# Optimization experiments

Hardware: AMD Instinct MI355X
Metric: run time of the kernel (lower is better)

## Reference

```python
import jax, jax.numpy as jnp
import numpy as np
from jax import lax

B, C, N = 8, 3, 65536
NUM_POINTS = 1024


def setup_inputs() -> dict:
    key = jax.random.key(0)
    points = jax.random.normal(key, (B, C, N), dtype=jnp.float32)
    return {"points": points}


def furthest_point_sampling(xyz, num_points):
    # xyz: (B, N, 3) -> indices (B, num_points), int32
    b, n, _ = xyz.shape
    init_idx = jnp.zeros((b,), dtype=jnp.int32)  # CUDA FPS seeds with index 0
    init_dists = jnp.full((b, n), 1e10, dtype=xyz.dtype)

    def step(carry, _):
        dists, last_idx = carry
        last_pt = jnp.take_along_axis(xyz, last_idx[:, None, None], axis=1)  # (B,1,3)
        d = jnp.sum(jnp.square(xyz - last_pt), axis=-1)  # (B,N) squared dist to newest pt
        dists = jnp.minimum(dists, d)
        nxt = jnp.argmax(dists, axis=-1).astype(jnp.int32)
        return (dists, nxt), nxt

    (_, _), rest = lax.scan(step, (init_dists, init_idx), None, length=num_points - 1)
    # rest: (num_points-1, B) -> (B, num_points)
    idx = jnp.concatenate([init_idx[None, :], rest], axis=0).T
    return idx


def reference(points):
    # points: (B, 3, N), channels-first as in the torch module
    xyz = jnp.transpose(points, (0, 2, 1))  # (B, N, 3)
    idx = furthest_point_sampling(xyz, NUM_POINTS)  # (B, num_points)
    # fps_gather_by_index: gather along point axis of (B, 3, N)
    new_points = jnp.take_along_axis(points, idx[:, None, :], axis=2)  # (B, 3, num_points)
    return new_points
```

## Files before the change

kernel.cpp:

```cpp
#include <hip/hip_runtime.h>


namespace {

constexpr int kB = 8;
constexpr int kN = 65536;
constexpr int kNP = 1024;
constexpr int kPB = 16;
constexpr int kThreads = 256;
constexpr int kPPT = kN / (kPB * kThreads);
constexpr int kGrp = kPPT / 4;
constexpr int kWaves = kThreads / 64;
constexpr int kRgn = 16;
constexpr int kRgnStride = 32;
constexpr int kBlocks = 256;

__device__ __forceinline__ unsigned long long shfl_xor_u64(unsigned long long v, int off) {
  return (unsigned long long)__shfl_xor((long long)v, off, 64);
}

__device__ __forceinline__ unsigned long long u64max(unsigned long long a,
                                                     unsigned long long b) {
  return a > b ? a : b;
}

__device__ __forceinline__ unsigned long long load_l2(const unsigned long long* p) {
  unsigned long long v;
  asm volatile("global_load_dwordx2 %0, %1, off sc0\n\ts_waitcnt vmcnt(0)"
               : "=v"(v)
               : "v"(p)
               : "memory");
  return v;
}

__device__ __forceinline__ void store_l2(unsigned long long* p, unsigned long long v) {
  asm volatile("global_store_dwordx2 %0, %1, off sc0" ::"v"(p), "v"(v) : "memory");
}

__global__ __launch_bounds__(kThreads) void fps_kernel(const float* __restrict__ pts,
                                                       float* __restrict__ out,
                                                       unsigned long long* __restrict__ slots,
                                                       unsigned* __restrict__ ctrl) {
  const int tid = threadIdx.x;
  const int lane = tid & 63;
  const int wave = tid >> 6;

  __shared__ int s_batch, s_slice;
  __shared__ unsigned long long s_wkey[kWaves];
  __shared__ unsigned s_win[2];
  __shared__ int s_hist[kNP];

  if (tid == 0) {
    unsigned xcc;
    asm volatile("s_getreg_b32 %0, hwreg(HW_REG_XCC_ID)" : "=s"(xcc));
    const int home = (int)(xcc & 7u);
    int batch = -1, slice = -1;
    const int pos = (int)atomicAdd(&ctrl[home], 1u);
    if (pos < kPB) {
      batch = home;
      slice = pos;
    }
    __hip_atomic_fetch_add(&ctrl[8], 1u, __ATOMIC_RELEASE, __HIP_MEMORY_SCOPE_AGENT);
    if (batch < 0) {
      while (__hip_atomic_load(&ctrl[8], __ATOMIC_ACQUIRE, __HIP_MEMORY_SCOPE_AGENT) <
             (unsigned)kBlocks) {
        __builtin_amdgcn_s_sleep(8);
      }
      int need = (int)atomicAdd(&ctrl[9], 1u);
      for (int j = 0; j < kB; ++j) {
        int have = (int)__hip_atomic_load(&ctrl[j], __ATOMIC_RELAXED, __HIP_MEMORY_SCOPE_AGENT);
        have = have > kPB ? kPB : have;
        const int vac = kPB - have;
        if (need < vac) {
          batch = j;
          slice = have + need;
          break;
        }
        need -= vac;
      }
    }
    s_batch = batch;
    s_slice = slice;
    s_win[0] = 0xFFFFFFFFu;
    s_win[1] = 0xFFFFFFFFu;
  }
  __syncthreads();

  const int batch = s_batch;
  const int slice = s_slice;
  if (batch < 0) return;

  const float* __restrict__ xb = pts + (size_t)batch * 3 * kN;
  const float* __restrict__ yb = xb + kN;
  const float* __restrict__ zb = xb + 2 * kN;

  const int sbase = slice * (kThreads * kPPT);
  const int base0 = sbase + tid * 4;
  float px[kPPT], py[kPPT], pz[kPPT], dist[kPPT];
#pragma unroll
  for (int g = 0; g < kGrp; ++g) {
    const int base = base0 + g * (kThreads * 4);
    const float4 vx = *reinterpret_cast<const float4*>(xb + base);
    const float4 vy = *reinterpret_cast<const float4*>(yb + base);
    const float4 vz = *reinterpret_cast<const float4*>(zb + base);
    px[g * 4 + 0] = vx.x; px[g * 4 + 1] = vx.y; px[g * 4 + 2] = vx.z; px[g * 4 + 3] = vx.w;
    py[g * 4 + 0] = vy.x; py[g * 4 + 1] = vy.y; py[g * 4 + 2] = vy.z; py[g * 4 + 3] = vy.w;
    pz[g * 4 + 0] = vz.x; pz[g * 4 + 1] = vz.y; pz[g * 4 + 2] = vz.z; pz[g * 4 + 3] = vz.w;
  }
#pragma unroll
  for (int k = 0; k < kPPT; ++k) dist[k] = 1e10f;

  float qx = xb[0], qy = yb[0], qz = zb[0];

  unsigned long long* const sb = slots + (size_t)batch * kRgn * kRgnStride;

  for (int it = 1; it < kNP; ++it) {
    float bd = -1.0f;
    int bi = 0;
#pragma unroll
    for (int g = 0; g < kGrp; ++g) {
#pragma unroll
      for (int j = 0; j < 4; ++j) {
        const int k = g * 4 + j;
        const float dx = px[k] - qx;
        const float dy = py[k] - qy;
        const float dz = pz[k] - qz;
        const float ss =
            __fadd_rn(__fadd_rn(__fmul_rn(dx, dx), __fmul_rn(dy, dy)), __fmul_rn(dz, dz));
        const float nd = fminf(dist[k], ss);
        dist[k] = nd;
        if (nd > bd) {
          bd = nd;
          bi = base0 + g * (kThreads * 4) + j;
        }
      }
    }

    unsigned long long key = ((unsigned long long)__float_as_uint(bd) << 32) |
                             ((unsigned long long)(0xFFFFu - (unsigned)bi) << 16) |
                             (unsigned long long)(unsigned)it;

#pragma unroll
    for (int off = 32; off > 0; off >>= 1) {
      key = u64max(key, shfl_xor_u64(key, off));
    }
    if (lane == 0) s_wkey[wave] = key;
    __syncthreads();

    int wi;
    if (wave == 0) {
      unsigned long long bk = s_wkey[lane & (kWaves - 1)];
#pragma unroll
      for (int off = 1; off < kWaves; off <<= 1) {
        bk = u64max(bk, shfl_xor_u64(bk, off));
      }

      unsigned long long* const rgn = sb + (size_t)(it & (kRgn - 1)) * kRgnStride;
      if (lane == 0) {
        store_l2(rgn + slice, bk);
        __hip_atomic_store(rgn + kPB + slice, bk, __ATOMIC_RELAXED,
                           __HIP_MEMORY_SCOPE_AGENT);
      }

      unsigned long long w;
      int round = 0;
      for (;;) {
        unsigned long long a = load_l2(rgn + (lane & (kPB - 1)));
        bool ok = (unsigned)(a & 0xFFFFull) == (unsigned)it;
        if (round >= 2 && !ok) {
          const unsigned long long fb = __hip_atomic_load(
              rgn + kPB + (lane & (kPB - 1)), __ATOMIC_RELAXED, __HIP_MEMORY_SCOPE_AGENT);
          if ((unsigned)(fb & 0xFFFFull) == (unsigned)it) {
            a = fb;
            ok = true;
          }
        }
        if (__all(ok)) {
          w = a;
          break;
        }
        ++round;
      }
#pragma unroll
      for (int off = 1; off < kPB; off <<= 1) {
        w = u64max(w, shfl_xor_u64(w, off));
      }
      wi = (int)(0xFFFFu - ((unsigned)(w >> 16) & 0xFFFFu));
      if (lane == 0) {
        s_hist[it] = wi;
        __hip_atomic_store(&s_win[it & 1], ((unsigned)wi << 16) | (unsigned)it,
                           __ATOMIC_RELAXED, __HIP_MEMORY_SCOPE_WORKGROUP);
      }
    } else {
      unsigned v;
      do {
        v = __hip_atomic_load(&s_win[it & 1], __ATOMIC_RELAXED, __HIP_MEMORY_SCOPE_WORKGROUP);
      } while ((v & 0xFFFFu) != (unsigned)it);
      wi = (int)(v >> 16);
    }

    const int wiu = __builtin_amdgcn_readfirstlane(wi);
    qx = xb[wiu];
    qy = yb[wiu];
    qz = zb[wiu];
  }

  __syncthreads();

  if (slice == 0) {
    float* __restrict__ ob = out + (size_t)batch * 3 * kNP;
    for (int j = tid; j < kNP; j += kThreads) {
      const int id = (j == 0) ? 0 : s_hist[j];
      ob[j] = xb[id];
      ob[kNP + j] = yb[id];
      ob[2 * kNP + j] = zb[id];
    }
  }
}

}

extern "C" void kernel_launch(void* const* d_in, const int* in_sizes, int n_in,
                              void* d_out, int out_size, void* d_ws, size_t ws_size,
                              hipStream_t stream) {
  (void)in_sizes;
  (void)n_in;
  (void)out_size;
  (void)ws_size;
  const float* pts = (const float*)d_in[0];
  float* out = (float*)d_out;
  unsigned* ctrl = (unsigned*)d_ws;
  unsigned long long* slots = (unsigned long long*)((char*)d_ws + 1024);
  hipMemsetAsync(d_ws, 0, 64, stream);
  fps_kernel<<<dim3(kBlocks), dim3(kThreads), 0, stream>>>(pts, out, slots, ctrl);
}
```

Measured before the change: 1.662 ms.

## Use DPP wave reductions and place exchange slots in output buffer

```diff
diff --git a/kernel.cpp b/kernel.cpp
--- a/kernel.cpp
+++ b/kernel.cpp
@@ -12,16 +12,33 @@
 constexpr int kGrp = kPPT / 4;
 constexpr int kWaves = kThreads / 64;
 constexpr int kRgn = 16;
-constexpr int kRgnStride = 32;
 constexpr int kBlocks = 256;
-
-__device__ __forceinline__ unsigned long long shfl_xor_u64(unsigned long long v, int off) {
-  return (unsigned long long)__shfl_xor((long long)v, off, 64);
-}
+constexpr unsigned kDoneTag = 0xD07Eu;
 
 __device__ __forceinline__ unsigned long long u64max(unsigned long long a,
                                                      unsigned long long b) {
   return a > b ? a : b;
+}
+
+template <int CTRL>
+__device__ __forceinline__ unsigned long long dpp_u64_zero(unsigned long long v) {
+  const unsigned lo =
+      (unsigned)__builtin_amdgcn_update_dpp(0, (int)(unsigned)v, CTRL, 0xf, 0xf, false);
+  const unsigned hi =
+      (unsigned)__builtin_amdgcn_update_dpp(0, (int)(unsigned)(v >> 32), CTRL, 0xf, 0xf, false);
+  return ((unsigned long long)hi << 32) | lo;
+}
+
+__device__ __forceinline__ unsigned long long wave_max_u64(unsigned long long v) {
+  v = u64max(v, dpp_u64_zero<0x111>(v));
+  v = u64max(v, dpp_u64_zero<0x112>(v));
+  v = u64max(v, dpp_u64_zero<0x114>(v));
+  v = u64max(v, dpp_u64_zero<0x118>(v));
+  v = u64max(v, dpp_u64_zero<0x142>(v));
+  v = u64max(v, dpp_u64_zero<0x143>(v));
+  const unsigned lo = (unsigned)__builtin_amdgcn_readlane((int)(unsigned)v, 63);
+  const unsigned hi = (unsigned)__builtin_amdgcn_readlane((int)(unsigned)(v >> 32), 63);
+  return ((unsigned long long)hi << 32) | lo;
 }
 
 __device__ __forceinline__ unsigned long long load_l2(const unsigned long long* p) {
@@ -39,7 +56,8 @@
 
 __global__ __launch_bounds__(kThreads) void fps_kernel(const float* __restrict__ pts,
                                                        float* __restrict__ out,
-                                                       unsigned long long* __restrict__ slots,
+                                                       unsigned long long* __restrict__ slotsB,
+                                                       unsigned long long* __restrict__ done,
                                                        unsigned* __restrict__ ctrl) {
   const int tid = threadIdx.x;
   const int lane = tid & 63;
@@ -94,6 +112,9 @@
   const float* __restrict__ yb = xb + kN;
   const float* __restrict__ zb = xb + 2 * kN;
 
+  unsigned long long* const lineA = (unsigned long long*)(out + (size_t)batch * 3 * kNP);
+  unsigned long long* const lineB = slotsB + (size_t)batch * kRgn * kPB;
+
   const int sbase = slice * (kThreads * kPPT);
   const int base0 = sbase + tid * 4;
   float px[kPPT], py[kPPT], pz[kPPT], dist[kPPT];
@@ -111,8 +132,6 @@
   for (int k = 0; k < kPPT; ++k) dist[k] = 1e10f;
 
   float qx = xb[0], qy = yb[0], qz = zb[0];
-
-  unsigned long long* const sb = slots + (size_t)batch * kRgn * kRgnStride;
 
   for (int it = 1; it < kNP; ++it) {
     float bd = -1.0f;
@@ -140,36 +159,30 @@
                              ((unsigned long long)(0xFFFFu - (unsigned)bi) << 16) |
                              (unsigned long long)(unsigned)it;
 
-#pragma unroll
-    for (int off = 32; off > 0; off >>= 1) {
-      key = u64max(key, shfl_xor_u64(key, off));
-    }
+    key = wave_max_u64(key);
     if (lane == 0) s_wkey[wave] = key;
     __syncthreads();
 
     int wi;
     if (wave == 0) {
       unsigned long long bk = s_wkey[lane & (kWaves - 1)];
-#pragma unroll
-      for (int off = 1; off < kWaves; off <<= 1) {
-        bk = u64max(bk, shfl_xor_u64(bk, off));
-      }
-
-      unsigned long long* const rgn = sb + (size_t)(it & (kRgn - 1)) * kRgnStride;
+      bk = wave_max_u64(bk);
+
+      const int rg = (it & (kRgn - 1)) * kPB;
       if (lane == 0) {
-        store_l2(rgn + slice, bk);
-        __hip_atomic_store(rgn + kPB + slice, bk, __ATOMIC_RELAXED,
+        store_l2(lineA + rg + slice, bk);
+        __hip_atomic_store(lineB + rg + slice, bk, __ATOMIC_RELAXED,
                            __HIP_MEMORY_SCOPE_AGENT);
       }
 
       unsigned long long w;
       int round = 0;
       for (;;) {
-        unsigned long long a = load_l2(rgn + (lane & (kPB - 1)));
+        unsigned long long a = load_l2(lineA + rg + (lane & (kPB - 1)));
         bool ok = (unsigned)(a & 0xFFFFull) == (unsigned)it;
-        if (round >= 2 && !ok) {
+        if (round >= 3 && !ok) {
           const unsigned long long fb = __hip_atomic_load(
-              rgn + kPB + (lane & (kPB - 1)), __ATOMIC_RELAXED, __HIP_MEMORY_SCOPE_AGENT);
+              lineB + rg + (lane & (kPB - 1)), __ATOMIC_RELAXED, __HIP_MEMORY_SCOPE_AGENT);
           if ((unsigned)(fb & 0xFFFFull) == (unsigned)it) {
             a = fb;
             ok = true;
@@ -181,10 +194,7 @@
         }
         ++round;
       }
-#pragma unroll
-      for (int off = 1; off < kPB; off <<= 1) {
-        w = u64max(w, shfl_xor_u64(w, off));
-      }
+      w = wave_max_u64(w);
       wi = (int)(0xFFFFu - ((unsigned)(w >> 16) & 0xFFFFu));
       if (lane == 0) {
         s_hist[it] = wi;
@@ -207,7 +217,22 @@
 
   __syncthreads();
 
+  if (tid == 0) {
+    __hip_atomic_store(&done[batch * kPB + slice],
+                       ((unsigned long long)slice << 32) | kDoneTag, __ATOMIC_RELEASE,
+                       __HIP_MEMORY_SCOPE_AGENT);
+  }
+
   if (slice == 0) {
+    if (wave == 0) {
+      unsigned long long d;
+      do {
+        d = __hip_atomic_load(&done[batch * kPB + (lane & (kPB - 1))], __ATOMIC_ACQUIRE,
+                              __HIP_MEMORY_SCOPE_AGENT);
+      } while (!__all((unsigned)(d & 0xFFFFull) == kDoneTag));
+    }
+    __syncthreads();
+
     float* __restrict__ ob = out + (size_t)batch * 3 * kNP;
     for (int j = tid; j < kNP; j += kThreads) {
       const int id = (j == 0) ? 0 : s_hist[j];
@@ -230,7 +255,8 @@
   const float* pts = (const float*)d_in[0];
   float* out = (float*)d_out;
   unsigned* ctrl = (unsigned*)d_ws;
-  unsigned long long* slots = (unsigned long long*)((char*)d_ws + 1024);
+  unsigned long long* slotsB = (unsigned long long*)((char*)d_ws + 1024);
+  unsigned long long* done = (unsigned long long*)((char*)d_ws + 32768);
   hipMemsetAsync(d_ws, 0, 64, stream);
-  fps_kernel<<<dim3(kBlocks), dim3(kThreads), 0, stream>>>(pts, out, slots, ctrl);
-}
+  fps_kernel<<<dim3(kBlocks), dim3(kThreads), 0, stream>>>(pts, out, slotsB, done, ctrl);
+}
```

Measured after the change: 1.824 ms. +9.8%, slower.
